# Performance work log

Measured on AMD Instinct MI355X. Metric: run time of the kernel, lower is better.

## Reference

```python
import jax, jax.numpy as jnp
import numpy as np

TEMPERATURE = 0.07
EPS = 1e-12  # matches torch F.normalize eps
B, D = 16384, 128


def setup_inputs() -> dict:
    key = jax.random.key(0)
    k1, k2 = jax.random.split(key)
    anchor = jax.random.normal(k1, (B, D), dtype=jnp.float32)
    positive = jax.random.normal(k2, (B, D), dtype=jnp.float32)
    return {"anchor": anchor, "positive": positive}


def _l2_normalize(x):
    # torch F.normalize: x / max(||x||, eps)
    n = jnp.sqrt(jnp.sum(x * x, axis=-1, keepdims=True))
    return x / jnp.maximum(n, EPS)


def reference(anchor, positive):
    a = _l2_normalize(anchor)          # [B, D]
    p = _l2_normalize(positive)        # [B, D]
    pos_sim = jnp.sum(a * p, axis=-1) / TEMPERATURE            # [B]
    sim = jnp.matmul(a, p.T) / TEMPERATURE                     # [B, B]
    neg_inf = jnp.finfo(sim.dtype).min
    bsz = sim.shape[0]
    eye = jnp.eye(bsz, dtype=bool)
    neg_sim = jnp.where(eye, neg_inf, sim)                     # diag masked
    logits = jnp.concatenate([pos_sim[:, None], neg_sim], axis=1)  # [B, B+1]
    # cross-entropy with label 0: -log_softmax(logits)[:, 0]
    lse = jax.nn.logsumexp(logits, axis=1)
    loss = lse - logits[:, 0]
    return jnp.mean(loss)
```

## Files before the change

### kernel.cpp

```cpp
#include <hip/hip_runtime.h>
#include <stdint.h>

#define NROWS 16384
#define DIM 128

typedef __attribute__((ext_vector_type(8))) __bf16 bf16x8;
typedef __attribute__((ext_vector_type(4))) float f32x4;
typedef __attribute__((ext_vector_type(4))) unsigned int u32x4;

constexpr float TEMP_INV = 1.0f / 0.07f;
constexpr float LOG2E = 1.4426950408889634f;
constexpr float LN2 = 0.69314718055994531f;
constexpr float KAPPA = LOG2E * TEMP_INV;
constexpr float SQRT_KAPPA = 4.53981600f;

__device__ __forceinline__ ushort f2bf(float x) {
  uint32_t u = __builtin_bit_cast(uint32_t, x);
  uint32_t r = (u + 0x7fffu + ((u >> 16) & 1u)) >> 16;
  return (ushort)r;
}

__device__ __forceinline__ void gload_lds16(const void* g, void* l) {
  __builtin_amdgcn_global_load_lds(
      (const __attribute__((address_space(1))) unsigned int*)g,
      (__attribute__((address_space(3))) unsigned int*)l, 16, 0, 0);
}

__global__ __launch_bounds__(256) void prep_kernel(
    const float* __restrict__ anchor, const float* __restrict__ positive,
    ushort* __restrict__ abar, ushort* __restrict__ pbar,
    float* __restrict__ pos_u)
{
  const int tid = threadIdx.x;
  const int row = blockIdx.x * 16 + (tid >> 4);
  const int c0 = (tid & 15) * 8;

  const float4* a4 = reinterpret_cast<const float4*>(anchor + (size_t)row * DIM + c0);
  const float4* p4 = reinterpret_cast<const float4*>(positive + (size_t)row * DIM + c0);
  float4 a0 = a4[0], a1 = a4[1];
  float4 p0 = p4[0], p1 = p4[1];

  float af[8] = {a0.x, a0.y, a0.z, a0.w, a1.x, a1.y, a1.z, a1.w};
  float pf[8] = {p0.x, p0.y, p0.z, p0.w, p1.x, p1.y, p1.z, p1.w};

  float sa = 0.f, sp = 0.f, dp = 0.f;
#pragma unroll
  for (int j = 0; j < 8; ++j) {
    sa += af[j] * af[j];
    sp += pf[j] * pf[j];
    dp += af[j] * pf[j];
  }
#pragma unroll
  for (int m = 1; m <= 8; m <<= 1) {
    sa += __shfl_xor(sa, m, 64);
    sp += __shfl_xor(sp, m, 64);
    dp += __shfl_xor(dp, m, 64);
  }
  float inva = 1.0f / fmaxf(sqrtf(sa), 1e-12f);
  float invp = 1.0f / fmaxf(sqrtf(sp), 1e-12f);
  float ca = inva * SQRT_KAPPA;
  float cp = invp * SQRT_KAPPA;

  ushort ua[8], up[8];
#pragma unroll
  for (int j = 0; j < 8; ++j) {
    ua[j] = f2bf(af[j] * ca);
    up[j] = f2bf(pf[j] * cp);
  }
  *reinterpret_cast<uint4*>(abar + (size_t)row * DIM + c0) = *reinterpret_cast<uint4*>(ua);
  *reinterpret_cast<uint4*>(pbar + (size_t)row * DIM + c0) = *reinterpret_cast<uint4*>(up);

  if ((tid & 15) == 0)
    pos_u[row] = dp * inva * invp * KAPPA;
}

#define NSPLIT 8
#define BM 256
#define CPB (NROWS / NSPLIT)
#define BN 32
#define NIT (CPB / BN)
#define NBUF 4

__global__ __launch_bounds__(512, 4) void lse_kernel(
    const ushort* __restrict__ abar,
    const ushort* __restrict__ pbar,
    float* __restrict__ sbuf )
{
  __shared__ alignas(16) char lds[NBUF][BN * 256];

  const int tid = threadIdx.x;
  const int l = tid & 63;
  const int w = tid >> 6;
  const int r15 = l & 15;
  const int hi = l >> 4;

  const int bid = blockIdx.x;
  const int csplit = bid & 7;
  const int rowblk = bid >> 3;
  const int row0 = rowblk * BM + w * 32;
  const int col0 = csplit * CPB;

  const char* abase = (const char*)abar;
  const char* pbase = (const char*)pbar;

  bf16x8 afrag[2][4];
#pragma unroll
  for (int rg = 0; rg < 2; ++rg)
#pragma unroll
    for (int kk = 0; kk < 4; ++kk) {
      size_t off = (size_t)(row0 + rg * 16 + r15) * 256 + (size_t)(kk * 32 + hi * 8) * 2;
      u32x4 v = *reinterpret_cast<const u32x4*>(abase + off);
      afrag[rg][kk] = __builtin_bit_cast(bf16x8, v);
    }

  float s[2][4];
#pragma unroll
  for (int rg = 0; rg < 2; ++rg)
#pragma unroll
    for (int rr = 0; rr < 4; ++rr) s[rg][rr] = 0.f;

  const int trow = w * 4 + (l >> 4);
  const size_t src0 = (size_t)(col0 + trow) * 256 + (size_t)(((l & 15) ^ (trow & 7)) * 16);
  void* ldst[NBUF];
#pragma unroll
  for (int b = 0; b < NBUF; ++b) ldst[b] = &lds[b][w * 1024];

  gload_lds16(pbase + src0, ldst[0]);
  __builtin_amdgcn_sched_barrier(0);
  gload_lds16(pbase + src0 + 8192, ldst[1]);
  __builtin_amdgcn_sched_barrier(0);

  for (int it = 0; it < NIT; ++it) {
    if (it < NIT - 1) {
      asm volatile("s_waitcnt vmcnt(1)" ::: "memory");
    } else {
      asm volatile("s_waitcnt vmcnt(0)" ::: "memory");
    }
    __builtin_amdgcn_s_barrier();
    asm volatile("" ::: "memory");
    __builtin_amdgcn_sched_barrier(0);

    if (it + 2 < NIT)
      gload_lds16(pbase + src0 + (size_t)(it + 2) * 8192, ldst[(it + 2) & 3]);

    const char* bufp = lds[it & 3];
#pragma unroll
    for (int ct = 0; ct < 2; ++ct) {
      const int tr = ct * 16 + r15;
      const int sw = (tr & 7) << 4;
      const char* base = bufp + tr * 256;
      bf16x8 bfrag[4];
#pragma unroll
      for (int kk = 0; kk < 4; ++kk) {
        const int cb = kk * 64 + hi * 16;
        u32x4 v = *reinterpret_cast<const u32x4*>(base + (cb ^ sw));
        bfrag[kk] = __builtin_bit_cast(bf16x8, v);
      }
      __builtin_amdgcn_s_setprio(1);
#pragma unroll
      for (int rg = 0; rg < 2; ++rg) {
        f32x4 acc = {0.f, 0.f, 0.f, 0.f};
#pragma unroll
        for (int kk = 0; kk < 4; ++kk)
          acc = __builtin_amdgcn_mfma_f32_16x16x32_bf16(afrag[rg][kk], bfrag[kk], acc, 0, 0, 0);
        s[rg][0] += __builtin_amdgcn_exp2f(acc[0]);
        s[rg][1] += __builtin_amdgcn_exp2f(acc[1]);
        s[rg][2] += __builtin_amdgcn_exp2f(acc[2]);
        s[rg][3] += __builtin_amdgcn_exp2f(acc[3]);
      }
      __builtin_amdgcn_s_setprio(0);
    }
  }

#pragma unroll
  for (int rg = 0; rg < 2; ++rg)
#pragma unroll
    for (int rr = 0; rr < 4; ++rr) {
      float v = s[rg][rr];
      v += __shfl_xor(v, 1, 64);
      v += __shfl_xor(v, 2, 64);
      v += __shfl_xor(v, 4, 64);
      v += __shfl_xor(v, 8, 64);
      if (r15 == 0) {
        int grow = row0 + rg * 16 + hi * 4 + rr;
        sbuf[(size_t)csplit * NROWS + grow] = v;
      }
    }
}

__global__ __launch_bounds__(256) void finalize1(
    const float* __restrict__ sbuf, const float* __restrict__ pos_u,
    float* __restrict__ partial)
{
  const int tid = threadIdx.x;
  const int r = blockIdx.x * 256 + tid;
  float ssum = 0.f;
#pragma unroll
  for (int c = 0; c < NSPLIT; ++c) ssum += sbuf[(size_t)c * NROWS + r];
  float acc = LN2 * (__builtin_amdgcn_logf(ssum) - pos_u[r]);
#pragma unroll
  for (int m = 1; m <= 32; m <<= 1) acc += __shfl_xor(acc, m, 64);
  __shared__ float red[4];
  if ((tid & 63) == 0) red[tid >> 6] = acc;
  __syncthreads();
  if (tid == 0) partial[blockIdx.x] = red[0] + red[1] + red[2] + red[3];
}

__global__ __launch_bounds__(64) void finalize2(
    const float* __restrict__ partial, float* __restrict__ out)
{
  float v = partial[threadIdx.x];
#pragma unroll
  for (int m = 1; m <= 32; m <<= 1) v += __shfl_xor(v, m, 64);
  if (threadIdx.x == 0) out[0] = v * (1.0f / (float)NROWS);
}

extern "C" void kernel_launch(void* const* d_in, const int* in_sizes, int n_in,
                              void* d_out, int out_size, void* d_ws, size_t ws_size,
                              hipStream_t stream) {
  const float* anchor = (const float*)d_in[0];
  const float* positive = (const float*)d_in[1];
  char* ws = (char*)d_ws;

  ushort* abar = (ushort*)ws;
  ushort* pbar = (ushort*)(ws + (size_t)NROWS * DIM * 2);
  float* pos_u = (float*)(ws + (size_t)NROWS * DIM * 4);
  float* sbuf = (float*)(ws + (size_t)NROWS * DIM * 4 + (size_t)NROWS * 4);
  float* partial = (float*)(ws + (size_t)NROWS * DIM * 4 + (size_t)NROWS * 4
                            + (size_t)NSPLIT * NROWS * 4);
  float* out = (float*)d_out;

  prep_kernel<<<NROWS / 16, 256, 0, stream>>>(anchor, positive, abar, pbar, pos_u);
  lse_kernel<<<NSPLIT * (NROWS / BM), 512, 0, stream>>>(abar, pbar, sbuf);
  finalize1<<<NROWS / 256, 256, 0, stream>>>(sbuf, pos_u, partial);
  finalize2<<<1, 64, 0, stream>>>(partial, out);
}
```

Baseline: 77.32 us.

## Enlarge per-wave tile to 64x32 with a 4x2 wave grid and BN=64

New measurement: 151.1 us. 1.95x slower.

```diff
diff --git a/kernel.cpp b/kernel.cpp
--- a/kernel.cpp
+++ b/kernel.cpp
@@ -77,35 +77,38 @@
 #define NSPLIT 8
 #define BM 256
 #define CPB (NROWS / NSPLIT)
-#define BN 32
+#define BN 64
 #define NIT (CPB / BN)
 #define NBUF 4
+#define TILE_B (BN * 256)
 
 __global__ __launch_bounds__(512, 4) void lse_kernel(
     const ushort* __restrict__ abar,
     const ushort* __restrict__ pbar,
     float* __restrict__ sbuf )
 {
-  __shared__ alignas(16) char lds[NBUF][BN * 256];
+  __shared__ alignas(16) char lds[NBUF][TILE_B];
 
   const int tid = threadIdx.x;
   const int l = tid & 63;
   const int w = tid >> 6;
+  const int wr = w >> 1;
+  const int wc = w & 1;
   const int r15 = l & 15;
   const int hi = l >> 4;
 
   const int bid = blockIdx.x;
   const int csplit = bid & 7;
   const int rowblk = bid >> 3;
-  const int row0 = rowblk * BM + w * 32;
+  const int row0 = rowblk * BM + wr * 64;
   const int col0 = csplit * CPB;
 
   const char* abase = (const char*)abar;
   const char* pbase = (const char*)pbar;
 
-  bf16x8 afrag[2][4];
-#pragma unroll
-  for (int rg = 0; rg < 2; ++rg)
+  bf16x8 afrag[4][4];
+#pragma unroll
+  for (int rg = 0; rg < 4; ++rg)
 #pragma unroll
     for (int kk = 0; kk < 4; ++kk) {
       size_t off = (size_t)(row0 + rg * 16 + r15) * 256 + (size_t)(kk * 32 + hi * 8) * 2;
@@ -113,26 +116,34 @@
       afrag[rg][kk] = __builtin_bit_cast(bf16x8, v);
     }
 
-  float s[2][4];
-#pragma unroll
-  for (int rg = 0; rg < 2; ++rg)
+  float s[4][4];
+#pragma unroll
+  for (int rg = 0; rg < 4; ++rg)
 #pragma unroll
     for (int rr = 0; rr < 4; ++rr) s[rg][rr] = 0.f;
 
   const int trow = w * 4 + (l >> 4);
   const size_t src0 = (size_t)(col0 + trow) * 256 + (size_t)(((l & 15) ^ (trow & 7)) * 16);
-  void* ldst[NBUF];
-#pragma unroll
-  for (int b = 0; b < NBUF; ++b) ldst[b] = &lds[b][w * 1024];
-
-  gload_lds16(pbase + src0, ldst[0]);
+  char* ldsw[NBUF];
+#pragma unroll
+  for (int b = 0; b < NBUF; ++b) ldsw[b] = &lds[b][w * 1024];
+
+#define STAGE(t)                                                              \
+  do {                                                                        \
+    const char* gsrc = pbase + src0 + (size_t)(t) * TILE_B;                   \
+    char* ld = ldsw[(t) & 3];                                                 \
+    gload_lds16(gsrc, ld);                                                    \
+    gload_lds16(gsrc + 8192, ld + 8192);                                      \
+  } while (0)
+
+  STAGE(0);
   __builtin_amdgcn_sched_barrier(0);
-  gload_lds16(pbase + src0 + 8192, ldst[1]);
+  STAGE(1);
   __builtin_amdgcn_sched_barrier(0);
 
   for (int it = 0; it < NIT; ++it) {
     if (it < NIT - 1) {
-      asm volatile("s_waitcnt vmcnt(1)" ::: "memory");
+      asm volatile("s_waitcnt vmcnt(2)" ::: "memory");
     } else {
       asm volatile("s_waitcnt vmcnt(0)" ::: "memory");
     }
@@ -140,13 +151,12 @@
     asm volatile("" ::: "memory");
     __builtin_amdgcn_sched_barrier(0);
 
-    if (it + 2 < NIT)
-      gload_lds16(pbase + src0 + (size_t)(it + 2) * 8192, ldst[(it + 2) & 3]);
+    if (it + 2 < NIT) STAGE(it + 2);
 
     const char* bufp = lds[it & 3];
 #pragma unroll
-    for (int ct = 0; ct < 2; ++ct) {
-      const int tr = ct * 16 + r15;
+    for (int ctg = 0; ctg < 2; ++ctg) {
+      const int tr = wc * 32 + ctg * 16 + r15;
       const int sw = (tr & 7) << 4;
       const char* base = bufp + tr * 256;
       bf16x8 bfrag[4];
@@ -158,7 +168,7 @@
       }
       __builtin_amdgcn_s_setprio(1);
 #pragma unroll
-      for (int rg = 0; rg < 2; ++rg) {
+      for (int rg = 0; rg < 4; ++rg) {
         f32x4 acc = {0.f, 0.f, 0.f, 0.f};
 #pragma unroll
         for (int kk = 0; kk < 4; ++kk)
@@ -171,9 +181,10 @@
       __builtin_amdgcn_s_setprio(0);
     }
   }
-
-#pragma unroll
-  for (int rg = 0; rg < 2; ++rg)
+#undef STAGE
+
+#pragma unroll
+  for (int rg = 0; rg < 4; ++rg)
 #pragma unroll
     for (int rr = 0; rr < 4; ++rr) {
       float v = s[rg][rr];
@@ -183,7 +194,7 @@
       v += __shfl_xor(v, 8, 64);
       if (r15 == 0) {
         int grow = row0 + rg * 16 + hi * 4 + rr;
-        sbuf[(size_t)csplit * NROWS + grow] = v;
+        sbuf[(size_t)(csplit * 2 + wc) * NROWS + grow] = v;
       }
     }
 }
@@ -196,7 +207,7 @@
   const int r = blockIdx.x * 256 + tid;
   float ssum = 0.f;
 #pragma unroll
-  for (int c = 0; c < NSPLIT; ++c) ssum += sbuf[(size_t)c * NROWS + r];
+  for (int c = 0; c < 2 * NSPLIT; ++c) ssum += sbuf[(size_t)c * NROWS + r];
   float acc = LN2 * (__builtin_amdgcn_logf(ssum) - pos_u[r]);
 #pragma unroll
   for (int m = 1; m <= 32; m <<= 1) acc += __shfl_xor(acc, m, 64);
@@ -227,7 +238,7 @@
   float* pos_u = (float*)(ws + (size_t)NROWS * DIM * 4);
   float* sbuf = (float*)(ws + (size_t)NROWS * DIM * 4 + (size_t)NROWS * 4);
   float* partial = (float*)(ws + (size_t)NROWS * DIM * 4 + (size_t)NROWS * 4
-                            + (size_t)NSPLIT * NROWS * 4);
+                            + (size_t)2 * NSPLIT * NROWS * 4);
   float* out = (float*)d_out;
 
   prep_kernel<<<NROWS / 16, 256, 0, stream>>>(anchor, positive, abar, pbar, pos_u);
```
